# Performance work log

Measured on AMD Instinct MI355X. Metric: run time of the kernel, lower is better.

## Reference

```python
import jax, jax.numpy as jnp
import numpy as np

GAMMA = 0.99
LAMDA = 0.95
EPS = 1e-8
T = 16777216  # number of steps


def setup_inputs() -> dict:
    key = jax.random.key(0)
    k1, k2, k3 = jax.random.split(key, 3)
    rewards = jax.random.normal(k1, (T,), dtype=jnp.float32)
    v_pred = jax.random.normal(k2, (T + 1,), dtype=jnp.float32)
    dones = jax.random.randint(k3, (T,), 0, 2, dtype=jnp.int32)
    return {"rewards": rewards, "v_pred": v_pred, "dones": dones}


def reference(rewards, v_pred, dones):
    not_done = 1.0 - dones.astype(rewards.dtype)  # [T]
    # TD residual with reset at done: delta_k = r_k + gamma*V_{k+1}*(1-done_k) - V_k
    delta = rewards + GAMMA * v_pred[1:] * not_done - v_pred[:-1]
    # continuation coefficient: adv_k = delta_k + gamma*lamda*(1-done_k)*adv_{k+1}
    cont = (GAMMA * LAMDA) * not_done

    def step(carry, xs):
        d, c = xs
        a = d + c * carry
        return a, a

    _, adv = jax.lax.scan(step, jnp.zeros((), rewards.dtype), (delta, cont), reverse=True)
    # standardize (stateless): (x - mean) / (std + eps)
    adv = (adv - jnp.mean(adv)) / (jnp.std(adv) + EPS)
    return adv
```

## Files before the change

kernel.cpp:

```cpp
#include <hip/hip_runtime.h>
#include <hip/hip_fp16.h>


#define GAMMA_F 0.99f
#define GL_F 0.9405f
#define EPS_F 1e-8f

constexpr int NT = 256;
constexpr int PL = 8;
constexpr int TILE = 512;
constexpr int CHUNK = 2 * TILE;
constexpr int K2T = 1024;

union H8 { __half h[8]; float4 f4; };

__device__ __forceinline__ void scan8(const float* d, const float* c, int lane,
                                      float& sD, float& sC, float& S1D, float& S1C) {
    float D = 0.f, C = 1.f;
#pragma unroll
    for (int i = 7; i >= 0; --i) { D = d[i] + c[i] * D; C *= c[i]; }
#pragma unroll
    for (int off = 1; off < 64; off <<= 1) {
        float tD = __shfl_down(D, off);
        float tC = __shfl_down(C, off);
        if (lane + off < 64) { D = D + C * tD; C = C * tC; }
    }
    sD = D; sC = C;
    S1D = __shfl_down(D, 1); S1C = __shfl_down(C, 1);
    if (lane == 63) { S1D = 0.f; S1C = 1.f; }
}

__device__ __forceinline__ void tile_scan(const float4& r0, const float4& r1,
                                          const float4& v0, const float4& v1,
                                          const float* nd, float vn63, int lane,
                                          float* d, float* c,
                                          float& sD, float& sC, float& S1D, float& S1C) {
    float vnext = __shfl_down(v0.x, 1);
    if (lane == 63) vnext = vn63;
    float va[9] = {v0.x, v0.y, v0.z, v0.w, v1.x, v1.y, v1.z, v1.w, vnext};
    float rf[8] = {r0.x, r0.y, r0.z, r0.w, r1.x, r1.y, r1.z, r1.w};
#pragma unroll
    for (int i = 0; i < 8; ++i) {
        d[i] = rf[i] + GAMMA_F * va[i + 1] * nd[i] - va[i];
        c[i] = GL_F * nd[i];
    }
    scan8(d, c, lane, sD, sC, S1D, S1C);
}

__device__ __forceinline__ void lane_moms(const float* d, const float* c,
                                          float S1D, float S1C, float* mm) {
    float x = S1D, P = S1C;
    float A = 0.f, Pp = 0.f, L2 = 0.f, LP = 0.f, P2 = 0.f;
#pragma unroll
    for (int i = 7; i >= 0; --i) {
        x = d[i] + c[i] * x;
        P *= c[i];
        A += x; Pp += P; L2 += x * x; LP += x * P; P2 += P * P;
    }
    mm[0] = A; mm[1] = Pp; mm[2] = L2; mm[3] = LP; mm[4] = P2;
}

__global__ __launch_bounds__(NT) void k_desc(const float* __restrict__ r,
                                             const float* __restrict__ v,
                                             const int* __restrict__ dn,
                                             float2* __restrict__ desc,
                                             float4* __restrict__ mom4,
                                             float* __restrict__ mom1,
                                             unsigned long long* __restrict__ dmask,
                                             __half* __restrict__ dh) {
    const int tid = threadIdx.x, lane = tid & 63, wv = tid >> 6;
    const int ch = blockIdx.x * 4 + wv;
    const int base = ch * CHUNK;
    const int o0 = base + lane * PL, o1 = base + TILE + lane * PL;

    float4 r00 = *(const float4*)(r + o0), r01 = *(const float4*)(r + o0 + 4);
    float4 v00 = *(const float4*)(v + o0), v01 = *(const float4*)(v + o0 + 4);
    int4   a00 = *(const int4*)(dn + o0),  a01 = *(const int4*)(dn + o0 + 4);
    float4 r10 = *(const float4*)(r + o1), r11 = *(const float4*)(r + o1 + 4);
    float4 v10 = *(const float4*)(v + o1), v11 = *(const float4*)(v + o1 + 4);
    int4   a10 = *(const int4*)(dn + o1),  a11 = *(const int4*)(dn + o1 + 4);

    float vn63_t1 = (lane == 63) ? v[base + CHUNK] : 0.f;
    float vn63_t0 = __shfl(v10.x, 0);

    int di0[8] = {a00.x, a00.y, a00.z, a00.w, a01.x, a01.y, a01.z, a01.w};
    int di1[8] = {a10.x, a10.y, a10.z, a10.w, a11.x, a11.y, a11.z, a11.w};
    float nd0[8], nd1[8];
    unsigned long long m0[8], m1[8];
#pragma unroll
    for (int i = 0; i < 8; ++i) {
        nd0[i] = 1.f - (float)di0[i]; m0[i] = __ballot(di0[i] != 0);
        nd1[i] = 1.f - (float)di1[i]; m1[i] = __ballot(di1[i] != 0);
    }

    float d1[8], c1[8], sD1, sC1, S1D1, S1C1;
    tile_scan(r10, r11, v10, v11, nd1, vn63_t1, lane, d1, c1, sD1, sC1, S1D1, S1C1);
    const float T1D = __shfl(sD1, 0), T1C = __shfl(sC1, 0);
    float d0[8], c0[8], sD0, sC0, S1D0, S1C0;
    tile_scan(r00, r01, v00, v01, nd0, vn63_t0, lane, d0, c0, sD0, sC0, S1D0, S1C0);
    const float T0D = __shfl(sD0, 0), T0C = __shfl(sC0, 0);

    H8 u0, u1;
#pragma unroll
    for (int i = 0; i < 8; ++i) { u0.h[i] = __float2half(d0[i]); u1.h[i] = __float2half(d1[i]); }
    *(float4*)(dh + o0) = u0.f4;
    *(float4*)(dh + o1) = u1.f4;

    float mm1[5], mm0[5];
    lane_moms(d1, c1, S1D1, S1C1, mm1);
    lane_moms(d0, c0, S1D0, S1C0, mm0);
    const float e = T1D, f = T1C;
    float gA  = mm1[0] + mm0[0] + e * mm0[1];
    float gP  = mm1[1] + f * mm0[1];
    float gL2 = mm1[2] + mm0[2] + 2.f * e * mm0[3] + e * e * mm0[4];
    float gLP = mm1[3] + f * (mm0[3] + e * mm0[4]);
    float gP2 = mm1[4] + f * f * mm0[4];
#pragma unroll
    for (int off = 32; off > 0; off >>= 1) {
        gA  += __shfl_down(gA,  off);
        gP  += __shfl_down(gP,  off);
        gL2 += __shfl_down(gL2, off);
        gLP += __shfl_down(gLP, off);
        gP2 += __shfl_down(gP2, off);
    }
    if (lane == 0) {
        desc[ch] = make_float2(T0D + T0C * T1D, T0C * T1C);
        mom4[ch] = make_float4(gA, gP, gL2, gLP);
        mom1[ch] = gP2;
        unsigned long long* mp = dmask + (size_t)ch * 16;
#pragma unroll
        for (int i = 0; i < 8; ++i) { mp[i] = m0[i]; mp[8 + i] = m1[i]; }
    }
}

__global__ __launch_bounds__(K2T) void k_scan(const float2* __restrict__ desc,
                                              const float4* __restrict__ mom4,
                                              const float* __restrict__ mom1,
                                              float* __restrict__ carry,
                                              float2* __restrict__ meanstd,
                                              int nchunk, long long T) {
    const int t = threadIdx.x, lane = t & 63, wv = t >> 6;
    const int per = nchunk / K2T;
    const int s = t * per;
    float D = 0.f, C = 1.f;
    for (int i = per - 1; i >= 0; --i) { float2 a = desc[s + i]; D = a.x + a.y * D; C *= a.y; }
    float sD = D, sC = C;
#pragma unroll
    for (int off = 1; off < 64; off <<= 1) {
        float tD = __shfl_down(sD, off), tC = __shfl_down(sC, off);
        if (lane + off < 64) { sD = sD + sC * tD; sC = sC * tC; }
    }
    __shared__ float2 waff[16];
    if (lane == 0) waff[wv] = make_float2(sD, sC);
    __syncthreads();
    float xw = 0.f;
    for (int w = 15; w > wv; --w) xw = waff[w].x + waff[w].y * xw;
    float S1D = __shfl_down(sD, 1), S1C = __shfl_down(sC, 1);
    if (lane == 63) { S1D = 0.f; S1C = 1.f; }
    float x = S1D + S1C * xw;
    double gS = 0.0, gQ = 0.0;
    for (int i = per - 1; i >= 0; --i) {
        const int cix = s + i;
        carry[cix] = x;
        float4 m = mom4[cix];
        float p2 = mom1[cix];
        gS += (double)(m.x + x * m.y);
        gQ += (double)(m.z + 2.f * x * m.w + x * x * p2);
        float2 a = desc[cix];
        x = a.x + a.y * x;
    }
#pragma unroll
    for (int off = 32; off > 0; off >>= 1) {
        gS += __shfl_down(gS, off);
        gQ += __shfl_down(gQ, off);
    }
    __shared__ double Sa[16], Sb[16];
    if (lane == 0) { Sa[wv] = gS; Sb[wv] = gQ; }
    __syncthreads();
    if (t == 0) {
        double S = 0.0, Q = 0.0;
        for (int w = 0; w < 16; ++w) { S += Sa[w]; Q += Sb[w]; }
        double mean = S / (double)T;
        double var = Q / (double)T - mean * mean;
        double sd = sqrt(var > 0.0 ? var : 0.0);
        meanstd[0] = make_float2((float)mean, (float)(1.0 / (sd + (double)EPS_F)));
    }
}

__global__ __launch_bounds__(NT) void k_apply(const __half* __restrict__ dh,
                                              const unsigned long long* __restrict__ dmask,
                                              const float* __restrict__ carry,
                                              const float2* __restrict__ meanstd,
                                              float* __restrict__ out) {
    const int tid = threadIdx.x, lane = tid & 63, wv = tid >> 6;
    const int ch = blockIdx.x * 4 + wv;
    const int base = ch * CHUNK;
    const int o0 = base + lane * PL, o1 = base + TILE + lane * PL;

    float d0[8], d1[8];
    H8 u0, u1;
    u0.f4 = *(const float4*)(dh + o0);
    u1.f4 = *(const float4*)(dh + o1);
#pragma unroll
    for (int i = 0; i < 8; ++i) { d0[i] = __half2float(u0.h[i]); d1[i] = __half2float(u1.h[i]); }

    const unsigned long long* mp = dmask + (size_t)ch * 16;
    float c0[8], c1[8];
#pragma unroll
    for (int i = 0; i < 8; ++i) {
        c0[i] = GL_F * (1.f - (float)((mp[i] >> lane) & 1ull));
        c1[i] = GL_F * (1.f - (float)((mp[8 + i] >> lane) & 1ull));
    }
    const float2 ms = meanstd[0];
    const float cy = carry[ch];

    float sD1, sC1, S1D1, S1C1;
    scan8(d1, c1, lane, sD1, sC1, S1D1, S1C1);
    const float T1D = __shfl(sD1, 0), T1C = __shfl(sC1, 0);
    float sD0, sC0, S1D0, S1C0;
    scan8(d0, c0, lane, sD0, sC0, S1D0, S1C0);

    float o[8];
    float x = S1D1 + S1C1 * cy;
#pragma unroll
    for (int i = 7; i >= 0; --i) { x = d1[i] + c1[i] * x; o[i] = (x - ms.x) * ms.y; }
    *(float4*)(out + o1)     = make_float4(o[0], o[1], o[2], o[3]);
    *(float4*)(out + o1 + 4) = make_float4(o[4], o[5], o[6], o[7]);
    const float x0e = T1D + T1C * cy;
    x = S1D0 + S1C0 * x0e;
#pragma unroll
    for (int i = 7; i >= 0; --i) { x = d0[i] + c0[i] * x; o[i] = (x - ms.x) * ms.y; }
    *(float4*)(out + o0)     = make_float4(o[0], o[1], o[2], o[3]);
    *(float4*)(out + o0 + 4) = make_float4(o[4], o[5], o[6], o[7]);
}

extern "C" void kernel_launch(void* const* d_in, const int* in_sizes, int n_in,
                              void* d_out, int out_size, void* d_ws, size_t ws_size,
                              hipStream_t stream) {
    const float* rewards = (const float*)d_in[0];
    const float* v_pred  = (const float*)d_in[1];
    const int*   dones   = (const int*)d_in[2];
    float* out = (float*)d_out;
    const long long T = in_sizes[0];
    const int nchunk = (int)(T / CHUNK);

    char* ws = (char*)d_ws;
    float4* mom4 = (float4*)ws;
    float2* desc = (float2*)(ws + (size_t)nchunk * 16);
    float*  mom1 = (float*)(ws + (size_t)nchunk * 24);
    float*  carry = (float*)(ws + (size_t)nchunk * 28);
    float2* meanstd = (float2*)(ws + (size_t)nchunk * 32);
    unsigned long long* dmask =
        (unsigned long long*)(ws + (size_t)nchunk * 32 + 16);
    __half* dh = (__half*)(ws + 4ull * 1024 * 1024);

    hipLaunchKernelGGL(k_desc, dim3(nchunk / 4), dim3(NT), 0, stream,
                       rewards, v_pred, dones, desc, mom4, mom1, dmask, dh);
    hipLaunchKernelGGL(k_scan, dim3(1), dim3(K2T), 0, stream,
                       desc, mom4, mom1, carry, meanstd, nchunk, T);
    hipLaunchKernelGGL(k_apply, dim3(nchunk / 4), dim3(NT), 0, stream,
                       dh, dmask, carry, meanstd, out);
}
```

Measured before the change: 107.8 us.

## Process contiguous 64-element segments per thread in descriptor kernel with software prefetch

The first pass is restructured so each thread walks a contiguous 64-element segment in float4 rounds, double-buffering its loads and folding the scan descriptor and the second-moment statistics serially. Lanes are then combined with a 16-lane shuffle scan, and each 16-lane group produces one 1024-element chunk descriptor. The done mask is now packed per thread as 64 bits, so the apply kernel decodes bytes in the new layout. The aim is fewer wavefronts, more memory-level parallelism per thread and fewer full-wave shuffles. In exchange, per-thread strided access across 256-byte segments may coalesce less well, and the 1024-block grid is small.

```diff
diff --git a/kernel.cpp b/kernel.cpp
--- a/kernel.cpp
+++ b/kernel.cpp
@@ -7,58 +7,15 @@
 #define EPS_F 1e-8f
 
 constexpr int NT = 256;
+constexpr int SEG = 64;
+constexpr int NRND = SEG / 4;
+constexpr int NBLK = 1024;
 constexpr int PL = 8;
 constexpr int TILE = 512;
-constexpr int CHUNK = 2 * TILE;
+constexpr int CHUNK = 1024;
 constexpr int K2T = 1024;
 
 union H8 { __half h[8]; float4 f4; };
-
-__device__ __forceinline__ void scan8(const float* d, const float* c, int lane,
-                                      float& sD, float& sC, float& S1D, float& S1C) {
-    float D = 0.f, C = 1.f;
-#pragma unroll
-    for (int i = 7; i >= 0; --i) { D = d[i] + c[i] * D; C *= c[i]; }
-#pragma unroll
-    for (int off = 1; off < 64; off <<= 1) {
-        float tD = __shfl_down(D, off);
-        float tC = __shfl_down(C, off);
-        if (lane + off < 64) { D = D + C * tD; C = C * tC; }
-    }
-    sD = D; sC = C;
-    S1D = __shfl_down(D, 1); S1C = __shfl_down(C, 1);
-    if (lane == 63) { S1D = 0.f; S1C = 1.f; }
-}
-
-__device__ __forceinline__ void tile_scan(const float4& r0, const float4& r1,
-                                          const float4& v0, const float4& v1,
-                                          const float* nd, float vn63, int lane,
-                                          float* d, float* c,
-                                          float& sD, float& sC, float& S1D, float& S1C) {
-    float vnext = __shfl_down(v0.x, 1);
-    if (lane == 63) vnext = vn63;
-    float va[9] = {v0.x, v0.y, v0.z, v0.w, v1.x, v1.y, v1.z, v1.w, vnext};
-    float rf[8] = {r0.x, r0.y, r0.z, r0.w, r1.x, r1.y, r1.z, r1.w};
-#pragma unroll
-    for (int i = 0; i < 8; ++i) {
-        d[i] = rf[i] + GAMMA_F * va[i + 1] * nd[i] - va[i];
-        c[i] = GL_F * nd[i];
-    }
-    scan8(d, c, lane, sD, sC, S1D, S1C);
-}
-
-__device__ __forceinline__ void lane_moms(const float* d, const float* c,
-                                          float S1D, float S1C, float* mm) {
-    float x = S1D, P = S1C;
-    float A = 0.f, Pp = 0.f, L2 = 0.f, LP = 0.f, P2 = 0.f;
-#pragma unroll
-    for (int i = 7; i >= 0; --i) {
-        x = d[i] + c[i] * x;
-        P *= c[i];
-        A += x; Pp += P; L2 += x * x; LP += x * P; P2 += P * P;
-    }
-    mm[0] = A; mm[1] = Pp; mm[2] = L2; mm[3] = LP; mm[4] = P2;
-}
 
 __global__ __launch_bounds__(NT) void k_desc(const float* __restrict__ r,
                                              const float* __restrict__ v,
@@ -66,70 +23,95 @@
                                              float2* __restrict__ desc,
                                              float4* __restrict__ mom4,
                                              float* __restrict__ mom1,
-                                             unsigned long long* __restrict__ dmask,
+                                             unsigned long long* __restrict__ dmask2,
                                              __half* __restrict__ dh) {
-    const int tid = threadIdx.x, lane = tid & 63, wv = tid >> 6;
-    const int ch = blockIdx.x * 4 + wv;
-    const int base = ch * CHUNK;
-    const int o0 = base + lane * PL, o1 = base + TILE + lane * PL;
-
-    float4 r00 = *(const float4*)(r + o0), r01 = *(const float4*)(r + o0 + 4);
-    float4 v00 = *(const float4*)(v + o0), v01 = *(const float4*)(v + o0 + 4);
-    int4   a00 = *(const int4*)(dn + o0),  a01 = *(const int4*)(dn + o0 + 4);
-    float4 r10 = *(const float4*)(r + o1), r11 = *(const float4*)(r + o1 + 4);
-    float4 v10 = *(const float4*)(v + o1), v11 = *(const float4*)(v + o1 + 4);
-    int4   a10 = *(const int4*)(dn + o1),  a11 = *(const int4*)(dn + o1 + 4);
-
-    float vn63_t1 = (lane == 63) ? v[base + CHUNK] : 0.f;
-    float vn63_t0 = __shfl(v10.x, 0);
-
-    int di0[8] = {a00.x, a00.y, a00.z, a00.w, a01.x, a01.y, a01.z, a01.w};
-    int di1[8] = {a10.x, a10.y, a10.z, a10.w, a11.x, a11.y, a11.z, a11.w};
-    float nd0[8], nd1[8];
-    unsigned long long m0[8], m1[8];
-#pragma unroll
-    for (int i = 0; i < 8; ++i) {
-        nd0[i] = 1.f - (float)di0[i]; m0[i] = __ballot(di0[i] != 0);
-        nd1[i] = 1.f - (float)di1[i]; m1[i] = __ballot(di1[i] != 0);
-    }
-
-    float d1[8], c1[8], sD1, sC1, S1D1, S1C1;
-    tile_scan(r10, r11, v10, v11, nd1, vn63_t1, lane, d1, c1, sD1, sC1, S1D1, S1C1);
-    const float T1D = __shfl(sD1, 0), T1C = __shfl(sC1, 0);
-    float d0[8], c0[8], sD0, sC0, S1D0, S1C0;
-    tile_scan(r00, r01, v00, v01, nd0, vn63_t0, lane, d0, c0, sD0, sC0, S1D0, S1C0);
-    const float T0D = __shfl(sD0, 0), T0C = __shfl(sC0, 0);
-
-    H8 u0, u1;
-#pragma unroll
-    for (int i = 0; i < 8; ++i) { u0.h[i] = __float2half(d0[i]); u1.h[i] = __float2half(d1[i]); }
-    *(float4*)(dh + o0) = u0.f4;
-    *(float4*)(dh + o1) = u1.f4;
-
-    float mm1[5], mm0[5];
-    lane_moms(d1, c1, S1D1, S1C1, mm1);
-    lane_moms(d0, c0, S1D0, S1C0, mm0);
-    const float e = T1D, f = T1C;
-    float gA  = mm1[0] + mm0[0] + e * mm0[1];
-    float gP  = mm1[1] + f * mm0[1];
-    float gL2 = mm1[2] + mm0[2] + 2.f * e * mm0[3] + e * e * mm0[4];
-    float gLP = mm1[3] + f * (mm0[3] + e * mm0[4]);
-    float gP2 = mm1[4] + f * f * mm0[4];
-#pragma unroll
-    for (int off = 32; off > 0; off >>= 1) {
-        gA  += __shfl_down(gA,  off);
-        gP  += __shfl_down(gP,  off);
-        gL2 += __shfl_down(gL2, off);
-        gLP += __shfl_down(gLP, off);
-        gP2 += __shfl_down(gP2, off);
-    }
-    if (lane == 0) {
-        desc[ch] = make_float2(T0D + T0C * T1D, T0C * T1C);
-        mom4[ch] = make_float4(gA, gP, gL2, gLP);
-        mom1[ch] = gP2;
-        unsigned long long* mp = dmask + (size_t)ch * 16;
-#pragma unroll
-        for (int i = 0; i < 8; ++i) { mp[i] = m0[i]; mp[8 + i] = m1[i]; }
+    const int tid = threadIdx.x, lane = tid & 63;
+    const int gtid = blockIdx.x * NT + tid;
+    const int wid = gtid >> 6;
+    const size_t e0 = (size_t)gtid * SEG;
+    const float4* rp = (const float4*)(r + e0);
+    const float4* vp = (const float4*)(v + e0);
+    const int4*   dp = (const int4*)(dn + e0);
+
+    float aD = 0.f, aC = 1.f, aA = 0.f, aP = 0.f, aL2 = 0.f, aLP = 0.f, aP2 = 0.f;
+    unsigned long long mbits = 0ull;
+    unsigned p01 = 0u, p23 = 0u;
+
+    float4 Rr[2], Vv[2]; int4 Dd[2]; float V4[2];
+    Rr[0] = rp[0]; Vv[0] = vp[0]; Dd[0] = dp[0]; V4[0] = v[e0 + 4];
+#pragma unroll
+    for (int t = 0; t < NRND; ++t) {
+        const int cur = t & 1, nxt = cur ^ 1;
+        if (t + 1 < NRND) {
+            Rr[nxt] = rp[t + 1]; Vv[nxt] = vp[t + 1]; Dd[nxt] = dp[t + 1];
+            V4[nxt] = v[e0 + 4 * (t + 1) + 4];
+        }
+        const float4 rr = Rr[cur], vv = Vv[cur];
+        const int4 dd = Dd[cur];
+        const float v4 = V4[cur];
+
+        const float nd0 = 1.f - (float)dd.x, nd1 = 1.f - (float)dd.y;
+        const float nd2 = 1.f - (float)dd.z, nd3 = 1.f - (float)dd.w;
+        const float d0 = rr.x + GAMMA_F * vv.y * nd0 - vv.x;
+        const float d1 = rr.y + GAMMA_F * vv.z * nd1 - vv.y;
+        const float d2 = rr.z + GAMMA_F * vv.w * nd2 - vv.z;
+        const float d3 = rr.w + GAMMA_F * v4   * nd3 - vv.w;
+        const float c0 = GL_F * nd0, c1 = GL_F * nd1, c2 = GL_F * nd2, c3 = GL_F * nd3;
+
+        const unsigned long long nib = (unsigned long long)((dd.x & 1) | ((dd.y & 1) << 1) |
+                                                            ((dd.z & 1) << 2) | ((dd.w & 1) << 3));
+        mbits |= nib << (4 * t);
+
+        __half2 h01 = __floats2half2_rn(d0, d1);
+        __half2 h23 = __floats2half2_rn(d2, d3);
+        const unsigned q01 = __builtin_bit_cast(unsigned, h01);
+        const unsigned q23 = __builtin_bit_cast(unsigned, h23);
+        if ((t & 1) == 0) { p01 = q01; p23 = q23; }
+        else {
+            *(uint4*)(dh + e0 + 4 * (t - 1)) = make_uint4(p01, p23, q01, q23);
+        }
+
+        float x = d3, P = c3;
+        float A = x, Pp = P, L2 = x * x, LP = x * P, P2 = P * P;
+        x = d2 + c2 * x; P *= c2; A += x; Pp += P; L2 += x * x; LP += x * P; P2 += P * P;
+        x = d1 + c1 * x; P *= c1; A += x; Pp += P; L2 += x * x; LP += x * P; P2 += P * P;
+        x = d0 + c0 * x; P *= c0; A += x; Pp += P; L2 += x * x; LP += x * P; P2 += P * P;
+        const float nA  = aA + x * aP + A;
+        const float nL2 = aL2 + 2.f * x * aLP + x * x * aP2 + L2;
+        const float nLP = P * (aLP + x * aP2) + LP;
+        const float nP2 = P * P * aP2 + P2;
+        const float nP  = P * aP + Pp;
+        const float nD  = aD + aC * x;
+        aC = aC * P; aD = nD;
+        aA = nA; aP = nP; aL2 = nL2; aLP = nLP; aP2 = nP2;
+    }
+    dmask2[gtid] = mbits;
+
+#pragma unroll
+    for (int off = 1; off < 16; off <<= 1) {
+        const float tD  = __shfl_down(aD,  off);
+        const float tC  = __shfl_down(aC,  off);
+        const float tA  = __shfl_down(aA,  off);
+        const float tP  = __shfl_down(aP,  off);
+        const float tL2 = __shfl_down(aL2, off);
+        const float tLP = __shfl_down(aLP, off);
+        const float tP2 = __shfl_down(aP2, off);
+        if ((lane & 15) + off < 16) {
+            const float nA  = aA + tD * aP + tA;
+            const float nL2 = aL2 + 2.f * tD * aLP + tD * tD * aP2 + tL2;
+            const float nLP = tC * (aLP + tD * aP2) + tLP;
+            const float nP2 = tC * tC * aP2 + tP2;
+            const float nP  = tC * aP + tP;
+            const float nD  = aD + aC * tD;
+            aC = aC * tC; aD = nD;
+            aA = nA; aP = nP; aL2 = nL2; aLP = nLP; aP2 = nP2;
+        }
+    }
+    if ((lane & 15) == 0) {
+        const int ch = wid * 4 + (lane >> 4);
+        desc[ch] = make_float2(aD, aC);
+        mom4[ch] = make_float4(aA, aP, aL2, aLP);
+        mom1[ch] = aP2;
     }
 }
 
@@ -187,8 +169,24 @@
     }
 }
 
+__device__ __forceinline__ void scan8(const float* d, const float* c, int lane,
+                                      float& sD, float& sC, float& S1D, float& S1C) {
+    float D = 0.f, C = 1.f;
+#pragma unroll
+    for (int i = 7; i >= 0; --i) { D = d[i] + c[i] * D; C *= c[i]; }
+#pragma unroll
+    for (int off = 1; off < 64; off <<= 1) {
+        float tD = __shfl_down(D, off);
+        float tC = __shfl_down(C, off);
+        if (lane + off < 64) { D = D + C * tD; C = C * tC; }
+    }
+    sD = D; sC = C;
+    S1D = __shfl_down(D, 1); S1C = __shfl_down(C, 1);
+    if (lane == 63) { S1D = 0.f; S1C = 1.f; }
+}
+
 __global__ __launch_bounds__(NT) void k_apply(const __half* __restrict__ dh,
-                                              const unsigned long long* __restrict__ dmask,
+                                              const unsigned long long* __restrict__ dmask2,
                                               const float* __restrict__ carry,
                                               const float2* __restrict__ meanstd,
                                               float* __restrict__ out) {
@@ -204,12 +202,13 @@
 #pragma unroll
     for (int i = 0; i < 8; ++i) { d0[i] = __half2float(u0.h[i]); d1[i] = __half2float(u1.h[i]); }
 
-    const unsigned long long* mp = dmask + (size_t)ch * 16;
+    const unsigned b0 = (unsigned)((dmask2[(size_t)ch * 16 + (lane >> 3)] >> ((lane & 7) * 8)) & 0xFFull);
+    const unsigned b1 = (unsigned)((dmask2[(size_t)ch * 16 + 8 + (lane >> 3)] >> ((lane & 7) * 8)) & 0xFFull);
     float c0[8], c1[8];
 #pragma unroll
     for (int i = 0; i < 8; ++i) {
-        c0[i] = GL_F * (1.f - (float)((mp[i] >> lane) & 1ull));
-        c1[i] = GL_F * (1.f - (float)((mp[8 + i] >> lane) & 1ull));
+        c0[i] = GL_F * (1.f - (float)((b0 >> i) & 1u));
+        c1[i] = GL_F * (1.f - (float)((b1 >> i) & 1u));
     }
     const float2 ms = meanstd[0];
     const float cy = carry[ch];
@@ -250,14 +249,14 @@
     float*  mom1 = (float*)(ws + (size_t)nchunk * 24);
     float*  carry = (float*)(ws + (size_t)nchunk * 28);
     float2* meanstd = (float2*)(ws + (size_t)nchunk * 32);
-    unsigned long long* dmask =
+    unsigned long long* dmask2 =
         (unsigned long long*)(ws + (size_t)nchunk * 32 + 16);
     __half* dh = (__half*)(ws + 4ull * 1024 * 1024);
 
-    hipLaunchKernelGGL(k_desc, dim3(nchunk / 4), dim3(NT), 0, stream,
-                       rewards, v_pred, dones, desc, mom4, mom1, dmask, dh);
+    hipLaunchKernelGGL(k_desc, dim3(NBLK), dim3(NT), 0, stream,
+                       rewards, v_pred, dones, desc, mom4, mom1, dmask2, dh);
     hipLaunchKernelGGL(k_scan, dim3(1), dim3(K2T), 0, stream,
                        desc, mom4, mom1, carry, meanstd, nchunk, T);
     hipLaunchKernelGGL(k_apply, dim3(nchunk / 4), dim3(NT), 0, stream,
-                       dh, dmask, carry, meanstd, out);
-}
+                       dh, dmask2, carry, meanstd, out);
+}
```

Measured after the change: 209.0 us. 1.94x slower.
